# Optimization experiments

Hardware: AMD Instinct MI355X
Metric: run time of the kernel (lower is better)

Reference implementation:

```python
import jax, jax.numpy as jnp
import numpy as np

LATENT, CTX, HID, TDIM, HEADS = 512, 512, 1024, 128, 8
HEAD_DIM = HID // HEADS
SCALE = HEAD_DIM ** -0.5


def _ln(x, g, b, eps=1e-5):
    m = jnp.mean(x, axis=-1, keepdims=True)
    v = jnp.mean((x - m) ** 2, axis=-1, keepdims=True)
    return (x - m) * jax.lax.rsqrt(v + eps) * g + b


def _time_embed(t):
    half = TDIM // 2
    exponent = jnp.linspace(0.0, 1.0, half, dtype=t.dtype)
    freqs = jnp.exp(jnp.log(1000.0) * exponent)
    ang = 2.0 * jnp.pi * t[:, None] * freqs[None, :]
    return jnp.concatenate([jnp.sin(ang), jnp.cos(ang)], axis=-1)  # [B, TDIM]


def setup_inputs() -> dict:
    key = jax.random.key(0)
    ks = iter(jax.random.split(key, 32))
    B, M = 4096, 64

    def w(k, i, o):
        return jax.random.normal(k, (i, o), jnp.float32) * 0.02

    inp = {
        "states": jax.random.normal(next(ks), (B, LATENT), jnp.float32),
        "time_values": jax.random.uniform(next(ks), (B,), jnp.float32),
        "class_summary": jax.random.normal(next(ks), (B, CTX), jnp.float32),
        "support_memory": jax.random.normal(next(ks), (B, M, LATENT), jnp.float32),
        # state_trunk: LN(latent+tdim) -> Linear -> GELU -> Linear
        "trunk_ln_g": jnp.ones((LATENT + TDIM,)), "trunk_ln_b": jnp.zeros((LATENT + TDIM,)),
        "trunk_w1": w(next(ks), LATENT + TDIM, HID), "trunk_b1": jnp.zeros((HID,)),
        "trunk_w2": w(next(ks), HID, HID), "trunk_b2": jnp.zeros((HID,)),
        # memory adapter: LN(latent) -> Linear(latent, hid)
        "mem_ln_g": jnp.ones((LATENT,)), "mem_ln_b": jnp.zeros((LATENT,)),
        "mem_w": w(next(ks), LATENT, HID), "mem_b": jnp.zeros((HID,)),
        # attention projections
        "wq": w(next(ks), HID, HID), "bq": jnp.zeros((HID,)),
        "wk": w(next(ks), HID, HID), "bk": jnp.zeros((HID,)),
        "wv": w(next(ks), HID, HID), "bv": jnp.zeros((HID,)),
        "wo": w(next(ks), HID, HID), "bo": jnp.zeros((HID,)),
        # pre-condition norm + FiLM
        "pre_ln_g": jnp.ones((HID,)), "pre_ln_b": jnp.zeros((HID,)),
        "film_w": w(next(ks), CTX, 2 * HID), "film_b": jnp.zeros((2 * HID,)),
        # conditioner: LN -> Linear -> GELU -> Linear
        "cond_ln_g": jnp.ones((HID,)), "cond_ln_b": jnp.zeros((HID,)),
        "cond_w1": w(next(ks), HID, HID), "cond_b1": jnp.zeros((HID,)),
        "cond_w2": w(next(ks), HID, HID), "cond_b2": jnp.zeros((HID,)),
        # output head: LN -> Linear -> GELU -> Linear(hid, latent)
        "head_ln_g": jnp.ones((HID,)), "head_ln_b": jnp.zeros((HID,)),
        "head_w1": w(next(ks), HID, HID), "head_b1": jnp.zeros((HID,)),
        "head_w2": w(next(ks), HID, LATENT), "head_b2": jnp.zeros((LATENT,)),
    }
    return inp


def _forward(states, time_values, class_summary, support_memory,
             trunk_ln_g, trunk_ln_b, trunk_w1, trunk_b1, trunk_w2, trunk_b2,
             mem_ln_g, mem_ln_b, mem_w, mem_b,
             wq, bq, wk, bk, wv, bv, wo, bo,
             pre_ln_g, pre_ln_b, film_w, film_b,
             cond_ln_g, cond_ln_b, cond_w1, cond_b1, cond_w2, cond_b2,
             head_ln_g, head_ln_b, head_w1, head_b1, head_w2, head_b2):
    B, M, _ = support_memory.shape
    gelu = lambda x: jax.nn.gelu(x, approximate=False)

    # trunk: g = Trunk([y, gamma(t)])
    te = _time_embed(time_values)
    x = _ln(jnp.concatenate([states, te], axis=-1), trunk_ln_g, trunk_ln_b)
    g = gelu(x @ trunk_w1 + trunk_b1) @ trunk_w2 + trunk_b2  # [B, HID]

    # encode memory + single-query multi-head attention
    mem_h = _ln(support_memory, mem_ln_g, mem_ln_b) @ mem_w + mem_b  # [B, M, HID]
    q = (g @ wq + bq).reshape(B, HEADS, HEAD_DIM)
    k = (mem_h @ wk + bk).reshape(B, M, HEADS, HEAD_DIM)
    v = (mem_h @ wv + bv).reshape(B, M, HEADS, HEAD_DIM)
    logits = jnp.einsum("bhd,bmhd->bhm", q, k) * SCALE
    attn = jax.nn.softmax(logits, axis=-1)
    summary = jnp.einsum("bhm,bmhd->bhd", attn, v).reshape(B, HID)
    attn_summary = summary @ wo + bo

    # FiLM conditioning
    combined = _ln(g + attn_summary, pre_ln_g, pre_ln_b)
    film = class_summary @ film_w + film_b
    scale, shift = film[:, :HID], film[:, HID:]
    combined = (1.0 + scale) * combined + shift
    cond_x = _ln(combined, cond_ln_g, cond_ln_b)
    conditioned = gelu(cond_x @ cond_w1 + cond_b1) @ cond_w2 + cond_b2 + combined

    # output head
    hx = _ln(conditioned, head_ln_g, head_ln_b)
    return gelu(hx @ head_w1 + head_b1) @ head_w2 + head_b2  # [B, LATENT]


def reference(states, time_values, class_summary, support_memory,
              trunk_ln_g, trunk_ln_b, trunk_w1, trunk_b1, trunk_w2, trunk_b2,
              mem_ln_g, mem_ln_b, mem_w, mem_b,
              wq, bq, wk, bk, wv, bv, wo, bo,
              pre_ln_g, pre_ln_b, film_w, film_b,
              cond_ln_g, cond_ln_b, cond_w1, cond_b1, cond_w2, cond_b2,
              head_ln_g, head_ln_b, head_w1, head_b1, head_w2, head_b2):
    return _forward(states, time_values, class_summary, support_memory,
                    trunk_ln_g, trunk_ln_b, trunk_w1, trunk_b1, trunk_w2, trunk_b2,
                    mem_ln_g, mem_ln_b, mem_w, mem_b,
                    wq, bq, wk, bk, wv, bv, wo, bo,
                    pre_ln_g, pre_ln_b, film_w, film_b,
                    cond_ln_g, cond_ln_b, cond_w1, cond_b1, cond_w2, cond_b2,
                    head_ln_g, head_ln_b, head_w1, head_b1, head_w2, head_b2)
```

## Files before the change

### kernel.cpp

```cpp
#include <hip/hip_runtime.h>
#include <cstdint>
#include <cstddef>

typedef unsigned short ushort_t;
typedef short s16x8 __attribute__((ext_vector_type(8)));
typedef float f32x4 __attribute__((ext_vector_type(4)));

__device__ __forceinline__ float bf2f(ushort_t h){
  union { unsigned int u; float f; } v; v.u = ((unsigned int)h) << 16; return v.f;
}
__device__ __forceinline__ ushort_t f2bf(float x){
  union { float f; unsigned int u; } v; v.f = x;
  unsigned int r = v.u + 0x7FFFu + ((v.u >> 16) & 1u);
  return (ushort_t)(r >> 16);
}
__device__ __forceinline__ float gelu_f(float x){
  return 0.5f * x * (1.0f + erff(x * 0.7071067811865475f));
}
__device__ __forceinline__ float wave_sum(float v){
  #pragma unroll
  for (int o = 32; o; o >>= 1) v += __shfl_xor(v, o);
  return v;
}
__device__ __forceinline__ void block_reduce2(float& s, float& q, float* red){
  s = wave_sum(s); q = wave_sum(q);
  int w = threadIdx.x >> 6, lane = threadIdx.x & 63, nw = blockDim.x >> 6;
  if (lane == 0){ red[w] = s; red[8 + w] = q; }
  __syncthreads();
  float ts = 0.f, tq = 0.f;
  for (int i = 0; i < nw; ++i){ ts += red[i]; tq += red[8 + i]; }
  __syncthreads();
  s = ts; q = tq;
}

#define SSLOT(cc, m) (((cc) & 56) | (((cc) & 7) ^ (((m) ^ ((m) >> 3)) & 7)))

struct TDesc { const float* in; ushort_t* out; int K; int N; int start; };
struct PrepArgs {
  const float* states; const float* tv; const float* lng; const float* lnb; ushort_t* xnb;
  TDesc t[11];
  int ntiles_end;
  int cast1_blocks;
  int cast_end;
  const float* memw; ushort_t* memwb;
  const float* csum; ushort_t* csb;
  const float* memb; const float* wv; const float* bvp; float* bv2;
};

__global__ __launch_bounds__(256) void prep_k(PrepArgs a){
  int bid = blockIdx.x, tid = threadIdx.x;
  __shared__ float buf[640];
  __shared__ float red[16];
  __shared__ float tbuf[32][33];
  if (bid < 4096){
    int row = bid;
    float t = a.tv[row];
    for (int i = tid; i < 640; i += 256){
      float v;
      if (i < 512) v = a.states[(size_t)row * 512 + i];
      else {
        int j = i - 512, jj = j & 63;
        float fr = expf(6.907755278982137f * ((float)jj * (1.0f / 63.0f)));
        float ang = 6.283185307179586f * t * fr;
        v = (j < 64) ? sinf(ang) : cosf(ang);
      }
      buf[i] = v;
    }
    __syncthreads();
    float s = 0.f, q = 0.f;
    for (int i = tid; i < 640; i += 256){ float v = buf[i]; s += v; q += v * v; }
    block_reduce2(s, q, red);
    float mean = s * (1.0f / 640.0f);
    float var = q * (1.0f / 640.0f) - mean * mean;
    float rstd = rsqrtf(var + 1e-5f);
    for (int i = tid; i < 640; i += 256)
      a.xnb[(size_t)row * 640 + i] = f2bf((buf[i] - mean) * rstd * a.lng[i] + a.lnb[i]);
    return;
  }
  bid -= 4096;
  if (bid < a.ntiles_end){
    int d = 0;
    #pragma unroll
    for (int i = 1; i < 11; ++i) if (bid >= a.t[i].start) d = i;
    TDesc td = a.t[d];
    int tile = bid - td.start;
    int tilesx = td.N >> 5;
    int n0 = (tile % tilesx) << 5, k0 = (tile / tilesx) << 5;
    int tx = tid & 31, ty = tid >> 5;
    #pragma unroll
    for (int j = 0; j < 32; j += 8)
      tbuf[ty + j][tx] = td.in[(size_t)(k0 + ty + j) * td.N + (n0 + tx)];
    __syncthreads();
    #pragma unroll
    for (int j = 0; j < 32; j += 8)
      td.out[(size_t)(n0 + ty + j) * td.K + (k0 + tx)] = f2bf(tbuf[tx][ty + j]);
  } else if (bid < a.cast_end){
    int ci = bid - a.ntiles_end;
    const float* src; ushort_t* dst; int i;
    if (ci < a.cast1_blocks){ src = a.memw; dst = a.memwb; i = ci * 1024 + tid * 4; }
    else { src = a.csum; dst = a.csb; i = (ci - a.cast1_blocks) * 1024 + tid * 4; }
    float4 v = *(const float4*)(src + i);
    union { ushort_t u[4]; uint2 p; } pk;
    pk.u[0] = f2bf(v.x); pk.u[1] = f2bf(v.y); pk.u[2] = f2bf(v.z); pk.u[3] = f2bf(v.w);
    *(uint2*)(dst + i) = pk.p;
  } else {
    int col = (bid - a.cast_end) * 256 + tid;
    float a0 = 0.f, a1 = 0.f, a2 = 0.f, a3 = 0.f;
    for (int j = 0; j < 1024; j += 4){
      a0 += a.memb[j + 0] * a.wv[(size_t)(j + 0) * 1024 + col];
      a1 += a.memb[j + 1] * a.wv[(size_t)(j + 1) * 1024 + col];
      a2 += a.memb[j + 2] * a.wv[(size_t)(j + 2) * 1024 + col];
      a3 += a.memb[j + 3] * a.wv[(size_t)(j + 3) * 1024 + col];
    }
    a.bv2[col] = a0 + a1 + a2 + a3 + a.bvp[col];
  }
}

__global__ __launch_bounds__(256) void ln_rows_k(const ushort_t* __restrict__ in, const float* __restrict__ g,
    const float* __restrict__ b, ushort_t* __restrict__ out, int D){
  int row = blockIdx.x, tid = threadIdx.x, i = tid * 4;
  __shared__ float red[16];
  union { uint2 p; ushort_t u[4]; } vv;
  vv.p = *(const uint2*)(in + (size_t)row * D + i);
  float v[4] = { bf2f(vv.u[0]), bf2f(vv.u[1]), bf2f(vv.u[2]), bf2f(vv.u[3]) };
  float s = v[0] + v[1] + v[2] + v[3];
  float q = v[0]*v[0] + v[1]*v[1] + v[2]*v[2] + v[3]*v[3];
  block_reduce2(s, q, red);
  float invD = 1.0f / (float)D;
  float mean = s * invD, var = q * invD - mean * mean, rstd = rsqrtf(var + 1e-5f);
  union { ushort_t u[4]; uint2 p; } pk;
  #pragma unroll
  for (int e = 0; e < 4; ++e) pk.u[e] = f2bf((v[e] - mean) * rstd * g[i + e] + b[i + e]);
  *(uint2*)(out + (size_t)row * D + i) = pk.p;
}

__global__ __launch_bounds__(256) void fuse_film_k(const ushort_t* __restrict__ combb, const ushort_t* __restrict__ filmb,
    const float* __restrict__ pg, const float* __restrict__ pb,
    const float* __restrict__ cg, const float* __restrict__ cb,
    ushort_t* __restrict__ c2b, ushort_t* __restrict__ cxb){
  int row = blockIdx.x, tid = threadIdx.x, i = tid * 4;
  __shared__ float red[16];
  union { uint2 p; ushort_t u[4]; } av;
  av.p = *(const uint2*)(combb + (size_t)row * 1024 + i);
  float x[4] = { bf2f(av.u[0]), bf2f(av.u[1]), bf2f(av.u[2]), bf2f(av.u[3]) };
  float s = x[0] + x[1] + x[2] + x[3];
  float q = x[0]*x[0] + x[1]*x[1] + x[2]*x[2] + x[3]*x[3];
  block_reduce2(s, q, red);
  float mean = s * (1.0f / 1024.0f), var = q * (1.0f / 1024.0f) - mean * mean;
  float rstd = rsqrtf(var + 1e-5f);
  float4 pgv = *(const float4*)(pg + i), pbv = *(const float4*)(pb + i);
  union { uint2 p; ushort_t u[4]; } scv, shv;
  scv.p = *(const uint2*)(filmb + (size_t)row * 2048 + i);
  shv.p = *(const uint2*)(filmb + (size_t)row * 2048 + 1024 + i);
  float c2[4];
  {
    float pgx[4] = { pgv.x, pgv.y, pgv.z, pgv.w };
    float pbx[4] = { pbv.x, pbv.y, pbv.z, pbv.w };
    #pragma unroll
    for (int e = 0; e < 4; ++e){
      float cc = (x[e] - mean) * rstd * pgx[e] + pbx[e];
      c2[e] = (1.0f + bf2f(scv.u[e])) * cc + bf2f(shv.u[e]);
    }
  }
  union { ushort_t u[4]; uint2 p; } pc;
  #pragma unroll
  for (int e = 0; e < 4; ++e) pc.u[e] = f2bf(c2[e]);
  *(uint2*)(c2b + (size_t)row * 1024 + i) = pc.p;
  float s2 = c2[0] + c2[1] + c2[2] + c2[3];
  float q2 = c2[0]*c2[0] + c2[1]*c2[1] + c2[2]*c2[2] + c2[3]*c2[3];
  block_reduce2(s2, q2, red);
  float m2 = s2 * (1.0f / 1024.0f), v2 = q2 * (1.0f / 1024.0f) - m2 * m2;
  float r2 = rsqrtf(v2 + 1e-5f);
  float4 cgv = *(const float4*)(cg + i), cbv = *(const float4*)(cb + i);
  union { ushort_t u[4]; uint2 p; } pk;
  pk.u[0] = f2bf((c2[0] - m2) * r2 * cgv.x + cbv.x);
  pk.u[1] = f2bf((c2[1] - m2) * r2 * cgv.y + cbv.y);
  pk.u[2] = f2bf((c2[2] - m2) * r2 * cgv.z + cbv.z);
  pk.u[3] = f2bf((c2[3] - m2) * r2 * cgv.w + cbv.w);
  *(uint2*)(cxb + (size_t)row * 1024 + i) = pk.p;
}

__global__ __launch_bounds__(256, 2) void suppattn_k(
    const float* __restrict__ support, const float* __restrict__ lgw, const float* __restrict__ lbw,
    const ushort_t* __restrict__ U, ushort_t* __restrict__ R)
{
  __shared__ ushort_t S[64 * 512];
  __shared__ ushort_t UG[9 * 512];
  __shared__ float WTf[8][65];
  __shared__ float SUMV[64], SUMSQ[64];
  __shared__ __align__(16) float MEANR[64];
  __shared__ __align__(16) float RSTDR[64];
  __shared__ float PMAX[4][8], PSUM[4][8], PMU[4][8];
  __shared__ float AB[2][8];
  __shared__ float MUH[8];

  int bb = blockIdx.x, tid = threadIdx.x, w = tid >> 6, l = tid & 63;
  const ushort_t* Ub = U + (size_t)bb * 4096;

  for (int id = tid; id < 576; id += 256){
    int hr8 = id >> 6, cc = id & 63;
    int byteoff = hr8 * 1024 + (((cc & 56) | ((cc & 7) ^ (hr8 & 7))) << 4);
    uint4* dst = (uint4*)((char*)UG + byteoff);
    if (hr8 < 8){
      s16x8 uv = *(const s16x8*)(Ub + hr8 * 512 + cc * 8);
      float4 g0 = *(const float4*)(lgw + cc * 8);
      float4 g1 = *(const float4*)(lgw + cc * 8 + 4);
      float ga[8] = { g0.x, g0.y, g0.z, g0.w, g1.x, g1.y, g1.z, g1.w };
      union { ushort_t u[8]; uint4 p; } pk;
      #pragma unroll
      for (int e = 0; e < 8; ++e) pk.u[e] = f2bf(ga[e] * bf2f((ushort_t)uv[e]));
      *dst = pk.p;
    } else {
      *dst = make_uint4(0x3F803F80u, 0x3F803F80u, 0x3F803F80u, 0x3F803F80u);
    }
  }

  {
    int h0 = 2 * w, h1 = 2 * w + 1;
    s16x8 u0 = *(const s16x8*)(Ub + h0 * 512 + l * 8);
    s16x8 u1 = *(const s16x8*)(Ub + h1 * 512 + l * 8);
    float4 g0 = *(const float4*)(lgw + l * 8), g1 = *(const float4*)(lgw + l * 8 + 4);
    float4 c0 = *(const float4*)(lbw + l * 8), c1 = *(const float4*)(lbw + l * 8 + 4);
    float ga[8] = { g0.x, g0.y, g0.z, g0.w, g1.x, g1.y, g1.z, g1.w };
    float ba[8] = { c0.x, c0.y, c0.z, c0.w, c1.x, c1.y, c1.z, c1.w };
    float A0 = 0.f, B0 = 0.f, A1 = 0.f, B1 = 0.f;
    #pragma unroll
    for (int e = 0; e < 8; ++e){
      float x0 = bf2f((ushort_t)u0[e]), x1 = bf2f((ushort_t)u1[e]);
      A0 += ba[e] * x0; B0 += ga[e] * x0;
      A1 += ba[e] * x1; B1 += ga[e] * x1;
    }
    A0 = wave_sum(A0); B0 = wave_sum(B0); A1 = wave_sum(A1); B1 = wave_sum(B1);
    if (l == 0){ AB[0][h0] = A0; AB[1][h0] = B0; AB[0][h1] = A1; AB[1][h1] = B1; }
  }

  #pragma unroll 4
  for (int i = 0; i < 16; ++i){
    int m = i * 4 + w;
    const float* row = support + ((size_t)bb * 64 + m) * 512 + l * 8;
    float4 a0 = *(const float4*)row, a1 = *(const float4*)(row + 4);
    union { ushort_t u[8]; uint4 p; } pk;
    pk.u[0] = f2bf(a0.x); pk.u[1] = f2bf(a0.y); pk.u[2] = f2bf(a0.z); pk.u[3] = f2bf(a0.w);
    pk.u[4] = f2bf(a1.x); pk.u[5] = f2bf(a1.y); pk.u[6] = f2bf(a1.z); pk.u[7] = f2bf(a1.w);
    int byteoff = m * 1024 + (SSLOT(l, m) << 4);
    *(uint4*)((char*)S + byteoff) = pk.p;
  }
  __syncthreads();

  int l15 = l & 15, lk = l >> 4;
  int hr = (l15 < 8) ? l15 : 8;
  int arowb = (w * 16 + l15) * 1024;
  int hrowb = hr * 1024;
  int am = w * 16 + l15;
  f32x4 dacc = (f32x4){0.f, 0.f, 0.f, 0.f};
  f32x4 sacc = (f32x4){0.f, 0.f, 0.f, 0.f};
  #pragma unroll
  for (int ks = 0; ks < 16; ++ks){
    int cc = ks * 4 + lk;
    s16x8 afr = *(const s16x8*)((char*)S + arowb + (SSLOT(cc, am) << 4));
    s16x8 bfr = *(const s16x8*)((char*)UG + hrowb + (((cc & 56) | ((cc & 7) ^ (hr & 7))) << 4));
    dacc = __builtin_amdgcn_mfma_f32_16x16x32_bf16(afr, bfr, dacc, 0, 0, 0);
    sacc = __builtin_amdgcn_mfma_f32_16x16x32_bf16(afr, afr, sacc, 0, 0, 0);
  }
  if (l15 == 8){
    #pragma unroll
    for (int j = 0; j < 4; ++j) SUMV[w * 16 + lk * 4 + j] = dacc[j];
  }
  if ((l15 >> 2) == lk) SUMSQ[w * 16 + l15] = sacc[l15 & 3];
  __syncthreads();
  if (tid < 64){
    float mean = SUMV[tid] * (1.0f / 512.0f);
    float var = SUMSQ[tid] * (1.0f / 512.0f) - mean * mean;
    MEANR[tid] = mean;
    RSTDR[tid] = rsqrtf(var + 1e-5f);
  }
  __syncthreads();

  int r0 = w * 16 + lk * 4;
  float4 mns = *(const float4*)(MEANR + r0);
  float4 rst = *(const float4*)(RSTDR + r0);
  float mn[4] = { mns.x, mns.y, mns.z, mns.w };
  float rs[4] = { rst.x, rst.y, rst.z, rst.w };
  float Ah = AB[0][l15 & 7], Bh = AB[1][l15 & 7];
  float lg[4];
  #pragma unroll
  for (int j = 0; j < 4; ++j)
    lg[j] = 0.08838834764831845f * (rs[j] * (dacc[j] - mn[j] * Bh) + Ah);
  float lmax = fmaxf(fmaxf(lg[0], lg[1]), fmaxf(lg[2], lg[3]));
  lmax = fmaxf(lmax, __shfl_xor(lmax, 16));
  lmax = fmaxf(lmax, __shfl_xor(lmax, 32));
  if (l < 8) PMAX[w][l] = lmax;
  __syncthreads();
  float gmax = fmaxf(fmaxf(PMAX[0][l15 & 7], PMAX[1][l15 & 7]),
                     fmaxf(PMAX[2][l15 & 7], PMAX[3][l15 & 7]));
  float e4[4]; float ls = 0.f, lm = 0.f;
  #pragma unroll
  for (int j = 0; j < 4; ++j){
    e4[j] = __expf(lg[j] - gmax);
    ls += e4[j];
    lm += e4[j] * rs[j] * mn[j];
  }
  ls += __shfl_xor(ls, 16); ls += __shfl_xor(ls, 32);
  lm += __shfl_xor(lm, 16); lm += __shfl_xor(lm, 32);
  if (l < 8){ PSUM[w][l] = ls; PMU[w][l] = lm; }
  __syncthreads();
  float Sh = PSUM[0][l15 & 7] + PSUM[1][l15 & 7] + PSUM[2][l15 & 7] + PSUM[3][l15 & 7];
  float inv = 1.0f / Sh;
  if (l15 < 8){
    #pragma unroll
    for (int j = 0; j < 4; ++j) WTf[l15][r0 + j] = e4[j] * rs[j] * inv;
  }
  if (w == 0 && l < 8){
    MUH[l] = (PMU[0][l] + PMU[1][l] + PMU[2][l] + PMU[3][l]) * inv;
  }
  __syncthreads();

  union { ushort_t u[8]; s16x8 v; } af0, af1;
  af0.v = (s16x8){0,0,0,0,0,0,0,0};
  af1.v = (s16x8){0,0,0,0,0,0,0,0};
  if (l15 < 8){
    #pragma unroll
    for (int e = 0; e < 8; ++e){
      af0.u[e] = f2bf(WTf[l15][lk * 8 + e]);
      af1.u[e] = f2bf(WTf[l15][32 + lk * 8 + e]);
    }
  }
  float mu[4];
  #pragma unroll
  for (int j = 0; j < 4; ++j) mu[j] = (lk < 2) ? MUH[lk * 4 + j] : 0.f;

  const char* Sp = (const char*)S;
  #pragma unroll
  for (int ns = 0; ns < 8; ++ns){
    int c = w * 128 + ns * 16 + l15;
    int cch = c >> 3, cb = (c & 7) * 2;
    int sb = cch & 56, cl = cch & 7;
    union { ushort_t u[8]; s16x8 v; } bf0, bf1;
    #pragma unroll
    for (int e = 0; e < 8; ++e){
      int m0 = lk * 8 + e;
      int m1 = m0 + 32;
      bf0.u[e] = *(const ushort_t*)(Sp + m0 * 1024 + ((sb | (cl ^ ((m0 ^ lk) & 7))) << 4) + cb);
      bf1.u[e] = *(const ushort_t*)(Sp + m1 * 1024 + ((sb | (cl ^ ((m1 ^ (4 + lk)) & 7))) << 4) + cb);
    }
    f32x4 cacc = (f32x4){0.f, 0.f, 0.f, 0.f};
    cacc = __builtin_amdgcn_mfma_f32_16x16x32_bf16(af0.v, bf0.v, cacc, 0, 0, 0);
    cacc = __builtin_amdgcn_mfma_f32_16x16x32_bf16(af1.v, bf1.v, cacc, 0, 0, 0);
    if (lk < 2){
      float gc = lgw[c], bc = lbw[c];
      #pragma unroll
      for (int j = 0; j < 4; ++j){
        int h = lk * 4 + j;
        R[(size_t)bb * 4096 + h * 512 + c] = f2bf(gc * (cacc[j] - mu[j]) + bc);
      }
    }
  }
}

#define GLL16(gsrc, ldst) \
  __builtin_amdgcn_global_load_lds((const __attribute__((address_space(1))) unsigned int*)(gsrc), \
                                   (__attribute__((address_space(3))) unsigned int*)(ldst), 16, 0, 0)

template<bool GELU, bool BIAS, bool WF32, bool WBF16, bool RESID>
__global__ __launch_bounds__(256, 3) void gemm_k(
    const ushort_t* __restrict__ A, int lda, long long aZ,
    const ushort_t* __restrict__ Bt, int ldb, long long bZ,
    const float* __restrict__ bias, long long biasZ,
    float* __restrict__ C, int ldc, long long cZ,
    ushort_t* __restrict__ Cb, int ldcb, long long cbZ,
    const ushort_t* __restrict__ R, int ldr,
    int M, int N, int K)
{
  __shared__ ushort_t smA[2][64 * 64];
  __shared__ ushort_t smB[2][128 * 64];
  int tid = threadIdx.x, lane = tid & 63, w = tid >> 6;
  int z = blockIdx.z;
  A  += (size_t)aZ * z;
  Bt += (size_t)bZ * z;
  if (BIAS)  bias += (size_t)biasZ * z;
  if (WF32)  C    += (size_t)cZ * z;
  if (WBF16) Cb   += (size_t)cbZ * z;

  int gx = gridDim.x, gy = gridDim.y;
  int nwg = gx * gy;
  int bx = blockIdx.x, by = blockIdx.y;
  if ((nwg & 7) == 0 && (gx & (gx - 1)) == 0){
    int lid = bx + gx * by;
    int cpx = nwg >> 3;
    int slid = (lid & 7) * cpx + (lid >> 3);
    int lgx = 31 - __clz(gx);
    bx = slid & (gx - 1);
    by = slid >> lgx;
  }
  int m0 = by * 64, n0 = bx * 128;
  int nk = K >> 6;

  auto stage = [&](int buf, int kt){
    int k0 = kt << 6;
    #pragma unroll
    for (int i = 0; i < 2; ++i){
      int c = ((w << 1) + i) * 64 + lane;
      int rowl = c >> 3, sp = c & 7;
      int sg = sp ^ (rowl & 7);
      GLL16(A + (size_t)(m0 + rowl) * lda + (k0 + sg * 8), &smA[buf][((w << 1) + i) * 512]);
    }
    #pragma unroll
    for (int i = 0; i < 4; ++i){
      int c = ((w << 2) + i) * 64 + lane;
      int rowl = c >> 3, sp = c & 7;
      int sg = sp ^ (rowl & 7);
      GLL16(Bt + (size_t)(n0 + rowl) * ldb + (k0 + sg * 8), &smB[buf][((w << 2) + i) * 512]);
    }
  };

  int qrow = w >> 1, qcol = w & 1;
  int l15 = lane & 15, lk = lane >> 4, l7 = lane & 7;
  int sb0 = ((0 + lk) ^ l7) << 4;
  int sb1 = ((4 + lk) ^ l7) << 4;
  int arow = (qrow * 32 + l15) * 128;
  int brow = (qcol * 64 + l15) * 128;

  f32x4 acc[2][4];
  #pragma unroll
  for (int m = 0; m < 2; ++m)
    #pragma unroll
    for (int n = 0; n < 4; ++n)
      acc[m][n] = (f32x4){0.f, 0.f, 0.f, 0.f};

  stage(0, 0);
  asm volatile("s_waitcnt vmcnt(0)" ::: "memory");
  __syncthreads();
  for (int kt = 0; kt < nk; ++kt){
    int cur = kt & 1;
    if (kt + 1 < nk) stage((kt + 1) & 1, kt + 1);
    const char* ab = (const char*)&smA[cur][0];
    const char* bbp = (const char*)&smB[cur][0];
    s16x8 af[2][2], bfv[4][2];
    #pragma unroll
    for (int m = 0; m < 2; ++m){
      af[m][0] = *(const s16x8*)(ab + arow + m * 2048 + sb0);
      af[m][1] = *(const s16x8*)(ab + arow + m * 2048 + sb1);
    }
    #pragma unroll
    for (int n = 0; n < 4; ++n){
      bfv[n][0] = *(const s16x8*)(bbp + brow + n * 2048 + sb0);
      bfv[n][1] = *(const s16x8*)(bbp + brow + n * 2048 + sb1);
    }
    #pragma unroll
    for (int kb = 0; kb < 2; ++kb)
      #pragma unroll
      for (int m = 0; m < 2; ++m)
        #pragma unroll
        for (int n = 0; n < 4; ++n)
          acc[m][n] = __builtin_amdgcn_mfma_f32_16x16x32_bf16(af[m][kb], bfv[n][kb], acc[m][n], 0, 0, 0);
    asm volatile("s_waitcnt vmcnt(0)" ::: "memory");
    __syncthreads();
  }

  #pragma unroll
  for (int n = 0; n < 4; ++n){
    int col = n0 + qcol * 64 + n * 16 + l15;
    float bvv = BIAS ? bias[col] : 0.0f;
    #pragma unroll
    for (int m = 0; m < 2; ++m){
      int rbase = m0 + qrow * 32 + m * 16 + lk * 4;
      #pragma unroll
      for (int r = 0; r < 4; ++r){
        float x = acc[m][n][r] + bvv;
        if (GELU) x = gelu_f(x);
        int row = rbase + r;
        if (RESID) x += bf2f(R[(size_t)row * ldr + col]);
        if (WF32)  C[(size_t)row * ldc + col] = x;
        if (WBF16) Cb[(size_t)row * ldcb + col] = f2bf(x);
      }
    }
  }
}

extern "C" void kernel_launch(void* const* d_in, const int* in_sizes, int n_in,
                              void* d_out, int out_size, void* d_ws, size_t ws_size,
                              hipStream_t stream)
{
  (void)in_sizes; (void)n_in; (void)out_size;
  const float* states      = (const float*)d_in[0];
  const float* time_values = (const float*)d_in[1];
  const float* class_sum   = (const float*)d_in[2];
  const float* support     = (const float*)d_in[3];
  const float* trunk_ln_g  = (const float*)d_in[4];
  const float* trunk_ln_b  = (const float*)d_in[5];
  const float* trunk_w1    = (const float*)d_in[6];
  const float* trunk_b1    = (const float*)d_in[7];
  const float* trunk_w2    = (const float*)d_in[8];
  const float* trunk_b2    = (const float*)d_in[9];
  const float* mem_ln_g    = (const float*)d_in[10];
  const float* mem_ln_b    = (const float*)d_in[11];
  const float* mem_w       = (const float*)d_in[12];
  const float* mem_b       = (const float*)d_in[13];
  const float* wq          = (const float*)d_in[14];
  const float* bq          = (const float*)d_in[15];
  const float* wk          = (const float*)d_in[16];
  const float* wv          = (const float*)d_in[18];
  const float* bvp         = (const float*)d_in[19];
  const float* wo          = (const float*)d_in[20];
  const float* bo          = (const float*)d_in[21];
  const float* pre_g       = (const float*)d_in[22];
  const float* pre_b       = (const float*)d_in[23];
  const float* film_w      = (const float*)d_in[24];
  const float* film_b      = (const float*)d_in[25];
  const float* cond_g      = (const float*)d_in[26];
  const float* cond_b      = (const float*)d_in[27];
  const float* cond_w1     = (const float*)d_in[28];
  const float* cond_b1     = (const float*)d_in[29];
  const float* cond_w2     = (const float*)d_in[30];
  const float* cond_b2     = (const float*)d_in[31];
  const float* head_g      = (const float*)d_in[32];
  const float* head_bb     = (const float*)d_in[33];
  const float* head_w1     = (const float*)d_in[34];
  const float* head_b1     = (const float*)d_in[35];
  const float* head_w2     = (const float*)d_in[36];
  const float* head_b2     = (const float*)d_in[37];
  float* out = (float*)d_out;

  char* ws = (char*)d_ws;
  size_t off = 0;
  auto alloc = [&](size_t bytes)->char*{
    char* p = ws + off;
    off += (bytes + 255) & ~(size_t)255;
    return p;
  };
  ushort_t* tw1T   = (ushort_t*)alloc((size_t)640 * 1024 * 2);
  ushort_t* tw2T   = (ushort_t*)alloc((size_t)1024 * 1024 * 2);
  ushort_t* wqT    = (ushort_t*)alloc((size_t)1024 * 1024 * 2);
  ushort_t* wkT    = (ushort_t*)alloc((size_t)1024 * 1024 * 2);
  ushort_t* wvT    = (ushort_t*)alloc((size_t)1024 * 1024 * 2);
  ushort_t* woT    = (ushort_t*)alloc((size_t)1024 * 1024 * 2);
  ushort_t* memw_b = (ushort_t*)alloc((size_t)512 * 1024 * 2);
  ushort_t* filmWT = (ushort_t*)alloc((size_t)512 * 2048 * 2);
  ushort_t* cw1T   = (ushort_t*)alloc((size_t)1024 * 1024 * 2);
  ushort_t* cw2T   = (ushort_t*)alloc((size_t)1024 * 1024 * 2);
  ushort_t* hw1T   = (ushort_t*)alloc((size_t)1024 * 1024 * 2);
  ushort_t* hw2T   = (ushort_t*)alloc((size_t)1024 * 512 * 2);
  ushort_t* K2     = (ushort_t*)alloc((size_t)512 * 1024 * 2);
  ushort_t* V2T    = (ushort_t*)alloc((size_t)1024 * 512 * 2);
  float*    bv2    = (float*)   alloc((size_t)1024 * 4);
  ushort_t* xnb    = (ushort_t*)alloc((size_t)4096 * 640 * 2);
  ushort_t* h1     = (ushort_t*)alloc((size_t)4096 * 1024 * 2);
  ushort_t* gb     = (ushort_t*)alloc((size_t)4096 * 1024 * 2);
  ushort_t* qb     = (ushort_t*)alloc((size_t)4096 * 1024 * 2);
  ushort_t* U      = (ushort_t*)alloc((size_t)4096 * 4096 * 2);
  ushort_t* Rb     = (ushort_t*)alloc((size_t)4096 * 4096 * 2);
  ushort_t* sumb   = (ushort_t*)alloc((size_t)4096 * 1024 * 2);
  ushort_t* combb  = (ushort_t*)alloc((size_t)4096 * 1024 * 2);
  ushort_t* csb    = (ushort_t*)alloc((size_t)4096 * 512 * 2);
  ushort_t* filmb  = (ushort_t*)alloc((size_t)4096 * 2048 * 2);
  ushort_t* c2b    = (ushort_t*)alloc((size_t)4096 * 1024 * 2);
  ushort_t* cxb    = (ushort_t*)alloc((size_t)4096 * 1024 * 2);
  ushort_t* c1     = (ushort_t*)alloc((size_t)4096 * 1024 * 2);
  ushort_t* cond2b = (ushort_t*)alloc((size_t)4096 * 1024 * 2);
  ushort_t* hxb    = (ushort_t*)alloc((size_t)4096 * 1024 * 2);
  ushort_t* h3     = (ushort_t*)alloc((size_t)4096 * 1024 * 2);
  if (off > ws_size) return;

  PrepArgs pa;
  pa.states = states; pa.tv = time_values; pa.lng = trunk_ln_g; pa.lnb = trunk_ln_b; pa.xnb = xnb;
  int s = 0;
  auto setT = [&](int i, const float* in, ushort_t* o, int K, int N){
    pa.t[i].in = in; pa.t[i].out = o; pa.t[i].K = K; pa.t[i].N = N; pa.t[i].start = s;
    s += (N >> 5) * (K >> 5);
  };
  setT(0, trunk_w1, tw1T, 640, 1024);
  setT(1, trunk_w2, tw2T, 1024, 1024);
  setT(2, wq, wqT, 1024, 1024);
  setT(3, wk, wkT, 1024, 1024);
  setT(4, wv, wvT, 1024, 1024);
  setT(5, wo, woT, 1024, 1024);
  setT(6, film_w, filmWT, 512, 2048);
  setT(7, cond_w1, cw1T, 1024, 1024);
  setT(8, cond_w2, cw2T, 1024, 1024);
  setT(9, head_w1, hw1T, 1024, 1024);
  setT(10, head_w2, hw2T, 1024, 512);
  pa.ntiles_end = s;
  pa.cast1_blocks = (512 * 1024) / 1024;
  pa.cast_end = s + pa.cast1_blocks + (4096 * 512) / 1024;
  pa.memw = mem_w; pa.memwb = memw_b;
  pa.csum = class_sum; pa.csb = csb;
  pa.memb = mem_b; pa.wv = wv; pa.bvp = bvp; pa.bv2 = bv2;
  prep_k<<<4096 + pa.cast_end + 4, 256, 0, stream>>>(pa);

  gemm_k<false, false, false, true, false><<<dim3(8, 8, 1), 256, 0, stream>>>(
      memw_b, 1024, 0, wkT, 1024, 0, nullptr, 0, nullptr, 0, 0, K2, 1024, 0, nullptr, 0, 512, 1024, 1024);
  gemm_k<false, false, false, true, false><<<dim3(4, 16, 1), 256, 0, stream>>>(
      wvT, 1024, 0, memw_b, 1024, 0, nullptr, 0, nullptr, 0, 0, V2T, 512, 0, nullptr, 0, 1024, 512, 1024);

  gemm_k<true, true, false, true, false><<<dim3(8, 64, 1), 256, 0, stream>>>(
      xnb, 640, 0, tw1T, 640, 0, trunk_b1, 0, nullptr, 0, 0, h1, 1024, 0, nullptr, 0, 4096, 1024, 640);
  gemm_k<false, true, false, true, false><<<dim3(8, 64, 1), 256, 0, stream>>>(
      h1, 1024, 0, tw2T, 1024, 0, trunk_b2, 0, nullptr, 0, 0, gb, 1024, 0, nullptr, 0, 4096, 1024, 1024);
  gemm_k<false, true, false, true, false><<<dim3(8, 64, 1), 256, 0, stream>>>(
      gb, 1024, 0, wqT, 1024, 0, bq, 0, nullptr, 0, 0, qb, 1024, 0, nullptr, 0, 4096, 1024, 1024);
  gemm_k<false, false, false, true, false><<<dim3(4, 64, 8), 256, 0, stream>>>(
      qb, 1024, 128, K2, 1024, 128, nullptr, 0, nullptr, 0, 0, U, 4096, 512, nullptr, 0, 4096, 512, 128);

  suppattn_k<<<4096, 256, 0, stream>>>(support, mem_ln_g, mem_ln_b, U, Rb);

  gemm_k<false, true, false, true, false><<<dim3(1, 64, 8), 256, 0, stream>>>(
      Rb, 4096, 512, V2T, 512, 65536, bv2, 128, nullptr, 0, 0, sumb, 1024, 128, nullptr, 0, 4096, 128, 512);

  gemm_k<false, true, false, true, true><<<dim3(8, 64, 1), 256, 0, stream>>>(
      sumb, 1024, 0, woT, 1024, 0, bo, 0, nullptr, 0, 0, combb, 1024, 0, gb, 1024, 4096, 1024, 1024);
  gemm_k<false, true, false, true, false><<<dim3(16, 64, 1), 256, 0, stream>>>(
      csb, 512, 0, filmWT, 512, 0, film_b, 0, nullptr, 0, 0, filmb, 2048, 0, nullptr, 0, 4096, 2048, 512);

  fuse_film_k<<<4096, 256, 0, stream>>>(combb, filmb, pre_g, pre_b, cond_g, cond_b, c2b, cxb);

  gemm_k<true, true, false, true, false><<<dim3(8, 64, 1), 256, 0, stream>>>(
      cxb, 1024, 0, cw1T, 1024, 0, cond_b1, 0, nullptr, 0, 0, c1, 1024, 0, nullptr, 0, 4096, 1024, 1024);
  gemm_k<false, true, false, true, true><<<dim3(8, 64, 1), 256, 0, stream>>>(
      c1, 1024, 0, cw2T, 1024, 0, cond_b2, 0, nullptr, 0, 0, cond2b, 1024, 0, c2b, 1024, 4096, 1024, 1024);
  ln_rows_k<<<4096, 256, 0, stream>>>(cond2b, head_g, head_bb, hxb, 1024);
  gemm_k<true, true, false, true, false><<<dim3(8, 64, 1), 256, 0, stream>>>(
      hxb, 1024, 0, hw1T, 1024, 0, head_b1, 0, nullptr, 0, 0, h3, 1024, 0, nullptr, 0, 4096, 1024, 1024);
  gemm_k<false, true, true, false, false><<<dim3(4, 64, 1), 256, 0, stream>>>(
      h3, 1024, 0, hw2T, 1024, 0, head_b2, 0, out, 512, 0, nullptr, 0, 0, nullptr, 0, 4096, 512, 1024);
}
```

Measured before the change: 451.8 us.

## Batch independent GEMMs into grouped launches and hoist support load in suppattn

```diff
diff --git a/kernel.cpp b/kernel.cpp
--- a/kernel.cpp
+++ b/kernel.cpp
@@ -197,6 +197,18 @@
   int bb = blockIdx.x, tid = threadIdx.x, w = tid >> 6, l = tid & 63;
   const ushort_t* Ub = U + (size_t)bb * 4096;
 
+  #pragma unroll 4
+  for (int i = 0; i < 16; ++i){
+    int m = i * 4 + w;
+    const float* row = support + ((size_t)bb * 64 + m) * 512 + l * 8;
+    float4 a0 = *(const float4*)row, a1 = *(const float4*)(row + 4);
+    union { ushort_t u[8]; uint4 p; } pk;
+    pk.u[0] = f2bf(a0.x); pk.u[1] = f2bf(a0.y); pk.u[2] = f2bf(a0.z); pk.u[3] = f2bf(a0.w);
+    pk.u[4] = f2bf(a1.x); pk.u[5] = f2bf(a1.y); pk.u[6] = f2bf(a1.z); pk.u[7] = f2bf(a1.w);
+    int byteoff = m * 1024 + (SSLOT(l, m) << 4);
+    *(uint4*)((char*)S + byteoff) = pk.p;
+  }
+
   for (int id = tid; id < 576; id += 256){
     int hr8 = id >> 6, cc = id & 63;
     int byteoff = hr8 * 1024 + (((cc & 56) | ((cc & 7) ^ (hr8 & 7))) << 4);
@@ -233,18 +245,6 @@
     A0 = wave_sum(A0); B0 = wave_sum(B0); A1 = wave_sum(A1); B1 = wave_sum(B1);
     if (l == 0){ AB[0][h0] = A0; AB[1][h0] = B0; AB[0][h1] = A1; AB[1][h1] = B1; }
   }
-
-  #pragma unroll 4
-  for (int i = 0; i < 16; ++i){
-    int m = i * 4 + w;
-    const float* row = support + ((size_t)bb * 64 + m) * 512 + l * 8;
-    float4 a0 = *(const float4*)row, a1 = *(const float4*)(row + 4);
-    union { ushort_t u[8]; uint4 p; } pk;
-    pk.u[0] = f2bf(a0.x); pk.u[1] = f2bf(a0.y); pk.u[2] = f2bf(a0.z); pk.u[3] = f2bf(a0.w);
-    pk.u[4] = f2bf(a1.x); pk.u[5] = f2bf(a1.y); pk.u[6] = f2bf(a1.z); pk.u[7] = f2bf(a1.w);
-    int byteoff = m * 1024 + (SSLOT(l, m) << 4);
-    *(uint4*)((char*)S + byteoff) = pk.p;
-  }
   __syncthreads();
 
   int l15 = l & 15, lk = l >> 4;
@@ -360,6 +360,114 @@
 #define GLL16(gsrc, ldst) \
   __builtin_amdgcn_global_load_lds((const __attribute__((address_space(1))) unsigned int*)(gsrc), \
                                    (__attribute__((address_space(3))) unsigned int*)(ldst), 16, 0, 0)
+
+struct GDesc {
+  const ushort_t* A; const ushort_t* Bt; const float* bias;
+  ushort_t* Cb; const ushort_t* R;
+  int lda, ldb, ldcb, ldr;
+  int gx, startBlock, flags, K;
+};
+struct GSet { GDesc d[3]; int nseg; };
+
+__global__ __launch_bounds__(256, 3) void gemmset_k(GSet gs){
+  __shared__ ushort_t smA[2][64 * 64];
+  __shared__ ushort_t smB[2][128 * 64];
+  int bid = blockIdx.x, tid = threadIdx.x, lane = tid & 63, w = tid >> 6;
+  int seg = 0;
+  #pragma unroll
+  for (int i = 1; i < 3; ++i) if (i < gs.nseg && bid >= gs.d[i].startBlock) seg = i;
+  GDesc g = gs.d[seg];
+  int lid = bid - g.startBlock;
+  {
+    int nwg = (seg + 1 < gs.nseg ? gs.d[seg + 1].startBlock : (int)gridDim.x) - g.startBlock;
+    int q = nwg >> 3;
+    lid = (lid & 7) * q + (lid >> 3);
+  }
+  int bx = lid % g.gx, by = lid / g.gx;
+  int m0 = by * 64, n0 = bx * 128;
+  int nk = g.K >> 6;
+
+  auto stage = [&](int buf, int kt){
+    int k0 = kt << 6;
+    #pragma unroll
+    for (int i = 0; i < 2; ++i){
+      int c = ((w << 1) + i) * 64 + lane;
+      int rowl = c >> 3, sp = c & 7;
+      int sg = sp ^ (rowl & 7);
+      GLL16(g.A + (size_t)(m0 + rowl) * g.lda + (k0 + sg * 8), &smA[buf][((w << 1) + i) * 512]);
+    }
+    #pragma unroll
+    for (int i = 0; i < 4; ++i){
+      int c = ((w << 2) + i) * 64 + lane;
+      int rowl = c >> 3, sp = c & 7;
+      int sg = sp ^ (rowl & 7);
+      GLL16(g.Bt + (size_t)(n0 + rowl) * g.ldb + (k0 + sg * 8), &smB[buf][((w << 2) + i) * 512]);
+    }
+  };
+
+  int qrow = w >> 1, qcol = w & 1;
+  int l15 = lane & 15, lk = lane >> 4, l7 = lane & 7;
+  int sb0 = ((0 + lk) ^ l7) << 4;
+  int sb1 = ((4 + lk) ^ l7) << 4;
+  int arow = (qrow * 32 + l15) * 128;
+  int brow = (qcol * 64 + l15) * 128;
+
+  f32x4 acc[2][4];
+  #pragma unroll
+  for (int m = 0; m < 2; ++m)
+    #pragma unroll
+    for (int n = 0; n < 4; ++n)
+      acc[m][n] = (f32x4){0.f, 0.f, 0.f, 0.f};
+
+  stage(0, 0);
+  asm volatile("s_waitcnt vmcnt(0)" ::: "memory");
+  __syncthreads();
+  for (int kt = 0; kt < nk; ++kt){
+    int cur = kt & 1;
+    if (kt + 1 < nk) stage((kt + 1) & 1, kt + 1);
+    const char* ab = (const char*)&smA[cur][0];
+    const char* bbp = (const char*)&smB[cur][0];
+    s16x8 af[2][2], bfv[4][2];
+    #pragma unroll
+    for (int m = 0; m < 2; ++m){
+      af[m][0] = *(const s16x8*)(ab + arow + m * 2048 + sb0);
+      af[m][1] = *(const s16x8*)(ab + arow + m * 2048 + sb1);
+    }
+    #pragma unroll
+    for (int n = 0; n < 4; ++n){
+      bfv[n][0] = *(const s16x8*)(bbp + brow + n * 2048 + sb0);
+      bfv[n][1] = *(const s16x8*)(bbp + brow + n * 2048 + sb1);
+    }
+    #pragma unroll
+    for (int kb = 0; kb < 2; ++kb)
+      #pragma unroll
+      for (int m = 0; m < 2; ++m)
+        #pragma unroll
+        for (int n = 0; n < 4; ++n)
+          acc[m][n] = __builtin_amdgcn_mfma_f32_16x16x32_bf16(af[m][kb], bfv[n][kb], acc[m][n], 0, 0, 0);
+    asm volatile("s_waitcnt vmcnt(0)" ::: "memory");
+    __syncthreads();
+  }
+
+  bool fGELU = g.flags & 1, fBIAS = g.flags & 2, fRES = g.flags & 16;
+  #pragma unroll
+  for (int n = 0; n < 4; ++n){
+    int col = n0 + qcol * 64 + n * 16 + l15;
+    float bvv = fBIAS ? g.bias[col] : 0.0f;
+    #pragma unroll
+    for (int m = 0; m < 2; ++m){
+      int rbase = m0 + qrow * 32 + m * 16 + lk * 4;
+      #pragma unroll
+      for (int r = 0; r < 4; ++r){
+        float x = acc[m][n][r] + bvv;
+        if (fGELU) x = gelu_f(x);
+        int row = rbase + r;
+        if (fRES) x += bf2f(g.R[(size_t)row * g.ldr + col]);
+        g.Cb[(size_t)row * g.ldcb + col] = f2bf(x);
+      }
+    }
+  }
+}
 
 template<bool GELU, bool BIAS, bool WF32, bool WBF16, bool RESID>
 __global__ __launch_bounds__(256, 3) void gemm_k(
@@ -587,17 +695,25 @@
   pa.memb = mem_b; pa.wv = wv; pa.bvp = bvp; pa.bv2 = bv2;
   prep_k<<<4096 + pa.cast_end + 4, 256, 0, stream>>>(pa);
 
-  gemm_k<false, false, false, true, false><<<dim3(8, 8, 1), 256, 0, stream>>>(
-      memw_b, 1024, 0, wkT, 1024, 0, nullptr, 0, nullptr, 0, 0, K2, 1024, 0, nullptr, 0, 512, 1024, 1024);
-  gemm_k<false, false, false, true, false><<<dim3(4, 16, 1), 256, 0, stream>>>(
-      wvT, 1024, 0, memw_b, 1024, 0, nullptr, 0, nullptr, 0, 0, V2T, 512, 0, nullptr, 0, 1024, 512, 1024);
-
-  gemm_k<true, true, false, true, false><<<dim3(8, 64, 1), 256, 0, stream>>>(
-      xnb, 640, 0, tw1T, 640, 0, trunk_b1, 0, nullptr, 0, 0, h1, 1024, 0, nullptr, 0, 4096, 1024, 640);
+  {
+    GSet gs; gs.nseg = 3;
+    gs.d[0] = { memw_b, wkT, nullptr, K2, nullptr, 1024, 1024, 1024, 0, 8, 0, 8, 1024 };
+    gs.d[1] = { wvT, memw_b, nullptr, V2T, nullptr, 1024, 1024, 512, 0, 4, 64, 8, 1024 };
+    gs.d[2] = { xnb, tw1T, trunk_b1, h1, nullptr, 640, 640, 1024, 0, 8, 128, 1|2|8, 640 };
+    gemmset_k<<<640, 256, 0, stream>>>(gs);
+  }
+
   gemm_k<false, true, false, true, false><<<dim3(8, 64, 1), 256, 0, stream>>>(
       h1, 1024, 0, tw2T, 1024, 0, trunk_b2, 0, nullptr, 0, 0, gb, 1024, 0, nullptr, 0, 4096, 1024, 1024);
-  gemm_k<false, true, false, true, false><<<dim3(8, 64, 1), 256, 0, stream>>>(
-      gb, 1024, 0, wqT, 1024, 0, bq, 0, nullptr, 0, 0, qb, 1024, 0, nullptr, 0, 4096, 1024, 1024);
+
+  {
+    GSet gs; gs.nseg = 2;
+    gs.d[0] = { gb, wqT, bq, qb, nullptr, 1024, 1024, 1024, 0, 8, 0, 2|8, 1024 };
+    gs.d[1] = { csb, filmWT, film_b, filmb, nullptr, 512, 512, 2048, 0, 16, 512, 2|8, 512 };
+    gs.d[2] = gs.d[1];
+    gemmset_k<<<1536, 256, 0, stream>>>(gs);
+  }
+
   gemm_k<false, false, false, true, false><<<dim3(4, 64, 8), 256, 0, stream>>>(
       qb, 1024, 128, K2, 1024, 128, nullptr, 0, nullptr, 0, 0, U, 4096, 512, nullptr, 0, 4096, 512, 128);
 
@@ -608,8 +724,6 @@
 
   gemm_k<false, true, false, true, true><<<dim3(8, 64, 1), 256, 0, stream>>>(
       sumb, 1024, 0, woT, 1024, 0, bo, 0, nullptr, 0, 0, combb, 1024, 0, gb, 1024, 4096, 1024, 1024);
-  gemm_k<false, true, false, true, false><<<dim3(16, 64, 1), 256, 0, stream>>>(
-      csb, 512, 0, filmWT, 512, 0, film_b, 0, nullptr, 0, 0, filmb, 2048, 0, nullptr, 0, 4096, 2048, 512);
 
   fuse_film_k<<<4096, 256, 0, stream>>>(combb, filmb, pre_g, pre_b, cond_g, cond_b, c2b, cxb);
 
```

New measurement: 414.8 us. 8.2% less time.
